# Kernel optimization log

Measured on AMD Instinct MI355X. Metric: run time of the kernel, lower is better.

The kernel has to match this reference:

```python
import jax, jax.numpy as jnp
import numpy as np

R = 0.4          # ball radius
K = 32           # max_neighbors
S = 512          # cluster_num
BN_EPS = 1e-5


def fps(data, npoint):
    """Furthest point sampling. data: [B,N,C] -> idx [B,npoint] int32.
    Deterministic start at index 0 (original uses randint)."""
    B, N, C = data.shape

    def step(carry, _):
        dist, far = carry
        cent = jnp.take_along_axis(data, far[:, None, None], axis=1)  # [B,1,C]
        d = jnp.sum((data - cent) ** 2, -1)                           # [B,N]
        dist = jnp.minimum(dist, d)
        new_far = jnp.argmax(dist, -1).astype(jnp.int32)
        return (dist, new_far), far

    dist0 = jnp.full((B, N), 1e10, data.dtype)
    far0 = jnp.zeros((B,), jnp.int32)
    _, idxs = jax.lax.scan(step, (dist0, far0), None, length=npoint)
    return idxs.T  # [B,npoint]


def gather_points(data, idx):
    """data [B,N,C], idx [B,S] -> [B,S,C]"""
    return jnp.take_along_axis(data, idx[..., None], axis=1)


def gather_groups(data, idx):
    """data [B,N,C], idx [B,S,K] -> [B,S,K,C]"""
    B, N, C = data.shape
    _, Sq, Kq = idx.shape
    flat = jnp.take_along_axis(data, idx.reshape(B, Sq * Kq)[..., None], axis=1)
    return flat.reshape(B, Sq, Kq, C)


def square_dist(a, b):
    """a [B,N,C], b [B,M,C] -> [B,N,M]"""
    return (-2.0 * jnp.einsum('bnc,bmc->bnm', a, b)
            + jnp.sum(a ** 2, -1)[:, :, None]
            + jnp.sum(b ** 2, -1)[:, None, :])


def knn_query(data, query, max_neighbors, r):
    """Ball query: indices of up to max_neighbors points within r, padded with
    the first valid index. data [B,N,C], query [B,S,C] -> [B,S,K] int32."""
    B, N, _ = data.shape
    d = square_dist(query, data)                              # [B,S,N]
    idx = jnp.where(d <= r * r, jnp.arange(N, dtype=jnp.int32)[None, None, :], N)
    idx = jnp.sort(idx, axis=-1)[:, :, :max_neighbors]        # ascending, N = invalid
    first = idx[:, :, :1]
    return jnp.where(idx == N, first, idx)


def mlp_layer(x, w, b, g, be):
    """1x1 Conv2d + BatchNorm2d (training-mode batch stats) + ReLU.
    x [B,S,K,Cin], w [Cout,Cin] -> [B,S,K,Cout]"""
    y = jnp.einsum('bskc,oc->bsko', x, w) + b
    m = jnp.mean(y, axis=(0, 1, 2))
    v = jnp.var(y, axis=(0, 1, 2))
    y = (y - m) * jax.lax.rsqrt(v + BN_EPS) * g + be
    return jax.nn.relu(y)


def setup_inputs() -> dict:
    key = jax.random.key(0)
    ks = jax.random.split(key, 5)
    B, N = 16, 8192
    data = jax.random.normal(ks[0], (B, N, 3), jnp.float32)
    data_feature = jax.random.normal(ks[1], (B, N, 3), jnp.float32)
    w0 = jax.random.normal(ks[2], (64, 6), jnp.float32) * 0.1
    w1 = jax.random.normal(ks[3], (64, 64), jnp.float32) * 0.1
    w2 = jax.random.normal(ks[4], (128, 64), jnp.float32) * 0.1
    zeros = lambda c: jnp.zeros((c,), jnp.float32)
    ones = lambda c: jnp.ones((c,), jnp.float32)
    return dict(data=data, data_feature=data_feature,
                w0=w0, b0=zeros(64), g0=ones(64), be0=zeros(64),
                w1=w1, b1=zeros(64), g1=ones(64), be1=zeros(64),
                w2=w2, b2=zeros(128), g2=ones(128), be2=zeros(128))


def reference(data, data_feature, w0, b0, g0, be0, w1, b1, g1, be1, w2, b2, g2, be2):
    B, N, C = data.shape
    fps_idx = fps(data, S)                              # [B,S]
    centroids = gather_points(data, fps_idx)            # [B,S,3]
    nbr_idx = knn_query(data, centroids, K, R)          # [B,S,K]
    sample = gather_groups(data, nbr_idx)               # [B,S,K,3]
    sample_norm = sample - centroids[:, :, None, :]
    feat = gather_groups(data_feature, nbr_idx)         # [B,S,K,3]
    x = jnp.concatenate([sample_norm, feat], axis=-1)   # [B,S,K,6]
    x = mlp_layer(x, w0, b0, g0, be0)
    x = mlp_layer(x, w1, b1, g1, be1)
    x = mlp_layer(x, w2, b2, g2, be2)
    out = jnp.max(x, axis=2)                            # [B,S,128]
    return centroids, out
```

## Files before the change

### kernel.cpp

```cpp
#include <hip/hip_runtime.h>
#include <math.h>

constexpr int Bc = 16;
constexpr int Nc = 8192;
constexpr int Sc = 512;
constexpr int Kc = 32;
constexpr int Pc = Bc * Sc * Kc;

typedef float v2f __attribute__((ext_vector_type(2)));

#if defined(__has_builtin)
#if __has_builtin(__builtin_elementwise_fma)
#define PKFMA(a, b, c) __builtin_elementwise_fma(a, b, c)
#endif
#endif
#ifndef PKFMA
__device__ __forceinline__ v2f pkfma_(v2f a, v2f b, v2f c) {
  v2f r; r.x = fmaf(a.x, b.x, c.x); r.y = fmaf(a.y, b.y, c.y); return r;
}
#define PKFMA(a, b, c) pkfma_(a, b, c)
#endif

template <int CTRL>
__device__ __forceinline__ float dpp_max_stage(float x) {
  int p = __builtin_amdgcn_update_dpp(0, __float_as_int(x), CTRL, 0xf, 0xf, true);
  return fmaxf(x, __int_as_float(p));
}

__global__ __launch_bounds__(256, 1)
void fps_kernel(const float* __restrict__ data,
                float* __restrict__ cent_out,
                float* __restrict__ cent_ws) {
  const int b = blockIdx.x;
  const int t = threadIdx.x;
  const int lane = t & 63, w = t >> 6;

  __shared__ float lx[Nc], ly[Nc], lz[Nc];
  __shared__ unsigned long long red_k[2][4];
  __shared__ int idx_hist[Sc];

  const float* db = data + (size_t)b * Nc * 3;

  float px[32], py[32], pz[32], dist[32];
#pragma unroll
  for (int j = 0; j < 32; ++j) {
    int p = t + 256 * j;
    px[j] = db[p * 3 + 0];
    py[j] = db[p * 3 + 1];
    pz[j] = db[p * 3 + 2];
    dist[j] = 1e10f;
    lx[p] = px[j]; ly[p] = py[j]; lz[p] = pz[j];
  }
  __syncthreads();

  int far = 0;
  for (int it = 0; it < Sc; ++it) {
    const int sfar = __builtin_amdgcn_readfirstlane(far);
    if (t == 0) idx_hist[it] = sfar;
    const float cx = lx[sfar];
    const float cy = ly[sfar];
    const float cz = lz[sfar];

    float best = -1.0f; int bj = 0;
#pragma unroll
    for (int j = 0; j < 32; ++j) {
      float dx = __fsub_rn(px[j], cx);
      float dy = __fsub_rn(py[j], cy);
      float dz = __fsub_rn(pz[j], cz);
      float d = __fadd_rn(__fadd_rn(__fmul_rn(dx, dx), __fmul_rn(dy, dy)),
                          __fmul_rn(dz, dz));
      float nd = fminf(dist[j], d);
      dist[j] = nd;
      if (nd > best) { best = nd; bj = j; }
    }
    const int bidx = t + 256 * bj;

    float wmax = best;
    wmax = dpp_max_stage<0xB1>(wmax);
    wmax = dpp_max_stage<0x4E>(wmax);
    wmax = dpp_max_stage<0x141>(wmax);
    wmax = dpp_max_stage<0x140>(wmax);
    wmax = fmaxf(wmax, __shfl_xor(wmax, 16));
    wmax = fmaxf(wmax, __shfl_xor(wmax, 32));

    unsigned long long m = __ballot(best == wmax);
    int idx;
    if (__popcll(m) == 1) {
      idx = __shfl(bidx, (int)__ffsll((long long)m) - 1);
    } else {
      int cand = (best == wmax) ? bidx : 0x7fffffff;
#pragma unroll
      for (int off = 32; off; off >>= 1) cand = min(cand, __shfl_xor(cand, off));
      idx = cand;
    }

    unsigned long long key =
        ((unsigned long long)__float_as_uint(wmax) << 32) |
        (unsigned long long)(0xFFFFFFFFu - (unsigned)idx);
    const int par = it & 1;
    if (lane == 0) red_k[par][w] = key;
    __syncthreads();

    unsigned long long k0 = red_k[par][0];
    unsigned long long k1 = red_k[par][1];
    unsigned long long k2 = red_k[par][2];
    unsigned long long k3 = red_k[par][3];
    unsigned long long ka = (k0 > k1) ? k0 : k1;
    unsigned long long kb = (k2 > k3) ? k2 : k3;
    unsigned long long kk = (ka > kb) ? ka : kb;
    far = (int)(0xFFFFFFFFu - (unsigned)(kk & 0xFFFFFFFFull));
  }

  __syncthreads();
  for (int s = t; s < Sc; s += 256) {
    int id = idx_hist[s];
    float vx = lx[id], vy = ly[id], vz = lz[id];
    size_t o = ((size_t)b * Sc + s) * 3;
    cent_out[o + 0] = vx; cent_out[o + 1] = vy; cent_out[o + 2] = vz;
    cent_ws[o + 0]  = vx; cent_ws[o + 1]  = vy; cent_ws[o + 2]  = vz;
  }
}

__global__ __launch_bounds__(256)
void ball_kernel(const float* __restrict__ data,
                 const float* __restrict__ feat,
                 const float* __restrict__ cent_ws,
                 const float* __restrict__ w0,
                 const float* __restrict__ b0,
                 float* __restrict__ x0,
                 float* __restrict__ part0) {
  const int w = threadIdx.x >> 6, lane = threadIdx.x & 63;
  const int t = threadIdx.x;
  const int q = blockIdx.x * 4 + w;
  const int b = q >> 9;
  const float* db = data + (size_t)b * Nc * 3;
  const float* fb = feat + (size_t)b * Nc * 3;

  const float qx = cent_ws[q * 3 + 0];
  const float qy = cent_ws[q * 3 + 1];
  const float qz = cent_ws[q * 3 + 2];
  const float q2 = __fadd_rn(__fadd_rn(__fmul_rn(qx, qx), __fmul_rn(qy, qy)),
                             __fmul_rn(qz, qz));

  __shared__ int nbr[4][Kc];
  __shared__ float x0s[6][128];
  int have = 0;
  for (int base = 0; base < Nc; base += 64) {
    int i = base + lane;
    float px = db[i * 3 + 0], py = db[i * 3 + 1], pz = db[i * 3 + 2];
    float p2 = __fadd_rn(__fadd_rn(__fmul_rn(px, px), __fmul_rn(py, py)),
                         __fmul_rn(pz, pz));
    float dt = fmaf(qz, pz, fmaf(qy, py, __fmul_rn(qx, px)));
    float d = __fadd_rn(__fadd_rn(__fmul_rn(-2.0f, dt), q2), p2);
    bool ok = d <= 0.16f;
    unsigned long long mask = __ballot(ok);
    if (mask) {
      int pos = have + __popcll(mask & ((1ull << lane) - 1ull));
      if (ok && pos < Kc) nbr[w][pos] = i;
      have += __popcll(mask);
      if (have >= Kc) break;
    }
  }
  if (have > Kc) have = Kc;
  __syncthreads();

  if (lane < Kc) {
    int k = lane;
    int j = nbr[w][k < have ? k : 0];
    float sx = __fsub_rn(db[j * 3 + 0], qx);
    float sy = __fsub_rn(db[j * 3 + 1], qy);
    float sz = __fsub_rn(db[j * 3 + 2], qz);
    float fx = fb[j * 3 + 0], fy = fb[j * 3 + 1], fz = fb[j * 3 + 2];
    size_t pidx = (size_t)q * Kc + k;
    x0[(size_t)0 * Pc + pidx] = sx;
    x0[(size_t)1 * Pc + pidx] = sy;
    x0[(size_t)2 * Pc + pidx] = sz;
    x0[(size_t)3 * Pc + pidx] = fx;
    x0[(size_t)4 * Pc + pidx] = fy;
    x0[(size_t)5 * Pc + pidx] = fz;
    int col = w * Kc + k;
    x0s[0][col] = sx; x0s[1][col] = sy; x0s[2][col] = sz;
    x0s[3][col] = fx; x0s[4][col] = fy; x0s[5][col] = fz;
  }
  __syncthreads();

  const int o = t & 63, q4 = t >> 6;
  float W[6];
#pragma unroll
  for (int c = 0; c < 6; ++c) W[c] = w0[o * 6 + c];
  const float bias = b0[o];
  float sum = 0.f, sq = 0.f;
#pragma unroll 4
  for (int k = 0; k < 32; ++k) {
    int p = q4 * 32 + k;
    float y = bias;
#pragma unroll
    for (int c = 0; c < 6; ++c) y = fmaf(x0s[c][p], W[c], y);
    sum += y;
    sq = fmaf(y, y, sq);
  }
  __shared__ float bsum[4][64], bsq[4][64];
  bsum[q4][o] = sum; bsq[q4][o] = sq;
  __syncthreads();
  if (t < 64)
    part0[blockIdx.x * 128 + t] =
        ((bsum[0][t] + bsum[1][t]) + bsum[2][t]) + bsum[3][t];
  else if (t < 128) {
    int oo = t - 64;
    part0[blockIdx.x * 128 + t] =
        ((bsq[0][oo] + bsq[1][oo]) + bsq[2][oo]) + bsq[3][oo];
  }
}

__global__ __launch_bounds__(256)
void reduce_k(const float* __restrict__ part, int nblk, int nch,
              const float* __restrict__ g, const float* __restrict__ be,
              float* __restrict__ AB) {
  const int o = blockIdx.x;
  const int t = threadIdx.x;
  double sum = 0.0, sq = 0.0;
  for (int i = t; i < nblk; i += 256) {
    sum += (double)part[(size_t)i * (2 * nch) + o];
    sq  += (double)part[(size_t)i * (2 * nch) + nch + o];
  }
  __shared__ double ls[256], lq[256];
  ls[t] = sum; lq[t] = sq;
  __syncthreads();
  for (int s = 128; s > 0; s >>= 1) {
    if (t < s) { ls[t] += ls[t + s]; lq[t] += lq[t + s]; }
    __syncthreads();
  }
  if (t == 0) {
    double m = ls[0] / (double)Pc;
    double v = lq[0] / (double)Pc - m * m;
    double A = (double)g[o] / sqrt(v + 1e-5);
    AB[o] = (float)A;
    AB[nch + o] = (float)((double)be[o] - m * A);
  }
}

__global__ __launch_bounds__(256)
void reduce2_final_k(const float* __restrict__ part, int nblk,
                     const float* __restrict__ g, const float* __restrict__ be,
                     const float* __restrict__ maxy2,
                     float* __restrict__ out) {
  const int o = blockIdx.x;
  const int t = threadIdx.x;
  double sum = 0.0, sq = 0.0;
  for (int i = t; i < nblk; i += 256) {
    sum += (double)part[(size_t)i * 256 + o];
    sq  += (double)part[(size_t)i * 256 + 128 + o];
  }
  __shared__ double ls[256], lq[256];
  ls[t] = sum; lq[t] = sq;
  __syncthreads();
  for (int s = 128; s > 0; s >>= 1) {
    if (t < s) { ls[t] += ls[t + s]; lq[t] += lq[t + s]; }
    __syncthreads();
  }
  __shared__ float sA, sB;
  if (t == 0) {
    double m = ls[0] / (double)Pc;
    double v = lq[0] / (double)Pc - m * m;
    double A = (double)g[o] / sqrt(v + 1e-5);
    sA = (float)A;
    sB = (float)((double)be[o] - m * A);
  }
  __syncthreads();
  const float A = sA, B = sB;
  for (int grp = t; grp < Bc * Sc; grp += 256) {
    float v = maxy2[(size_t)grp * 128 + o];
    out[(size_t)grp * 128 + o] = fmaxf(fmaf(v, A, B), 0.f);
  }
}

__global__ __launch_bounds__(256)
void pass_b(const float* __restrict__ x0, const float* __restrict__ w0,
            const float* __restrict__ b0, const float* __restrict__ AB0,
            const float* __restrict__ w1, const float* __restrict__ b1,
            float* __restrict__ y1, float* __restrict__ part1) {
  const int p = blockIdx.x * 256 + threadIdx.x;
  const int lane = threadIdx.x & 63, w = threadIdx.x >> 6;

  float xin[6];
#pragma unroll
  for (int c = 0; c < 6; ++c) xin[c] = x0[(size_t)c * Pc + p];

  float x1s[64];
#pragma unroll
  for (int o = 0; o < 64; ++o) {
    float y = b0[o];
#pragma unroll
    for (int c = 0; c < 6; ++c) y = fmaf(xin[c], w0[o * 6 + c], y);
    x1s[o] = fmaxf(fmaf(y, AB0[o], AB0[64 + o]), 0.f);
  }
  v2f x1p[32];
#pragma unroll
  for (int j = 0; j < 32; ++j) { x1p[j].x = x1s[2 * j]; x1p[j].y = x1s[2 * j + 1]; }

  const v2f* __restrict__ w1v = (const v2f*)w1;

  __shared__ float ssum[4][64][17], ssq[4][64][17];

  for (int o = 0; o < 64; ++o) {
    v2f a01; a01.x = b1[o]; a01.y = 0.f;
    v2f a23; a23.x = 0.f;   a23.y = 0.f;
#pragma unroll
    for (int c2 = 0; c2 < 32; c2 += 2) {
      a01 = PKFMA(x1p[c2 + 0], w1v[o * 32 + c2 + 0], a01);
      a23 = PKFMA(x1p[c2 + 1], w1v[o * 32 + c2 + 1], a23);
    }
    float acc = (a01.x + a01.y) + (a23.x + a23.y);
    y1[(size_t)o * Pc + p] = acc;

    float sv = acc + __shfl_xor(acc, 1);
    sv += __shfl_xor(sv, 2);
    float q = acc * acc;
    float qv = q + __shfl_xor(q, 1);
    qv += __shfl_xor(qv, 2);
    if ((lane & 3) == 0) {
      ssum[w][o][lane >> 2] = sv;
      ssq[w][o][lane >> 2] = qv;
    }
  }
  __syncthreads();
  if (threadIdx.x < 128) {
    const int o = threadIdx.x & 63;
    const bool isq = threadIdx.x >= 64;
    float s = 0.f;
#pragma unroll
    for (int ww = 0; ww < 4; ++ww)
      for (int k = 0; k < 16; ++k)
        s += isq ? ssq[ww][o][k] : ssum[ww][o][k];
    part1[blockIdx.x * 128 + threadIdx.x] = s;
  }
}

__global__ __launch_bounds__(256)
void pass_c(const float* __restrict__ y1, const float* __restrict__ AB1,
            const float* __restrict__ w2, const float* __restrict__ b2,
            float* __restrict__ maxy2, float* __restrict__ part2) {
  const int p = blockIdx.x * 256 + threadIdx.x;
  const int lane = threadIdx.x & 63, w = threadIdx.x >> 6;
  const int grp = p >> 5;

  v2f x2p[32];
#pragma unroll
  for (int c = 0; c < 64; c += 2) {
    float v0 = y1[(size_t)c * Pc + p];
    float v1 = y1[(size_t)(c + 1) * Pc + p];
    x2p[c >> 1].x = fmaxf(fmaf(v0, AB1[c], AB1[64 + c]), 0.f);
    x2p[c >> 1].y = fmaxf(fmaf(v1, AB1[c + 1], AB1[64 + c + 1]), 0.f);
  }

  const v2f* __restrict__ w2v = (const v2f*)w2;

  __shared__ float ssum[4][128][9], ssq[4][128][9];

  for (int o = 0; o < 128; ++o) {
    v2f a01; a01.x = b2[o]; a01.y = 0.f;
    v2f a23; a23.x = 0.f;   a23.y = 0.f;
#pragma unroll
    for (int c2 = 0; c2 < 32; c2 += 2) {
      a01 = PKFMA(x2p[c2 + 0], w2v[o * 32 + c2 + 0], a01);
      a23 = PKFMA(x2p[c2 + 1], w2v[o * 32 + c2 + 1], a23);
    }
    float acc = (a01.x + a01.y) + (a23.x + a23.y);

    float mx = acc;
#pragma unroll
    for (int off = 16; off > 0; off >>= 1) mx = fmaxf(mx, __shfl_xor(mx, off));
    if ((lane & 31) == 0) maxy2[(size_t)grp * 128 + o] = mx;

    float sv = acc + __shfl_xor(acc, 1);
    sv += __shfl_xor(sv, 2);
    sv += __shfl_xor(sv, 4);
    float q = acc * acc;
    float qv = q + __shfl_xor(q, 1);
    qv += __shfl_xor(qv, 2);
    qv += __shfl_xor(qv, 4);
    if ((lane & 7) == 0) {
      ssum[w][o][lane >> 3] = sv;
      ssq[w][o][lane >> 3] = qv;
    }
  }
  __syncthreads();
  {
    const int o = threadIdx.x & 127;
    const bool isq = threadIdx.x >= 128;
    float s = 0.f;
#pragma unroll
    for (int ww = 0; ww < 4; ++ww)
      for (int k = 0; k < 8; ++k)
        s += isq ? ssq[ww][o][k] : ssum[ww][o][k];
    part2[blockIdx.x * 256 + threadIdx.x] = s;
  }
}

extern "C" void kernel_launch(void* const* d_in, const int* in_sizes, int n_in,
                              void* d_out, int out_size, void* d_ws, size_t ws_size,
                              hipStream_t stream) {
  const float* data = (const float*)d_in[0];
  const float* feat = (const float*)d_in[1];
  const float* w0 = (const float*)d_in[2];
  const float* b0 = (const float*)d_in[3];
  const float* g0 = (const float*)d_in[4];
  const float* be0 = (const float*)d_in[5];
  const float* w1 = (const float*)d_in[6];
  const float* b1 = (const float*)d_in[7];
  const float* g1 = (const float*)d_in[8];
  const float* be1 = (const float*)d_in[9];
  const float* w2 = (const float*)d_in[10];
  const float* b2 = (const float*)d_in[11];
  const float* g2 = (const float*)d_in[12];
  const float* be2 = (const float*)d_in[13];
  float* out = (float*)d_out;

  float* ws = (float*)d_ws;
  float* cent_ws = ws; ws += (size_t)Bc * Sc * 3;
  float* x0 = ws;      ws += (size_t)6 * Pc;
  float* y1 = ws;      ws += (size_t)64 * Pc;
  float* maxy2 = ws;   ws += (size_t)Bc * Sc * 128;
  float* part0 = ws;   ws += 2048 * 128;
  float* part1 = ws;   ws += 1024 * 128;
  float* part2 = ws;   ws += 1024 * 256;
  float* AB0 = ws;     ws += 128;
  float* AB1 = ws;     ws += 128;

  fps_kernel<<<Bc, 256, 0, stream>>>(data, out, cent_ws);
  ball_kernel<<<(Bc * Sc) / 4, 256, 0, stream>>>(data, feat, cent_ws,
                                                 w0, b0, x0, part0);
  reduce_k<<<64, 256, 0, stream>>>(part0, 2048, 64, g0, be0, AB0);
  pass_b<<<Pc / 256, 256, 0, stream>>>(x0, w0, b0, AB0, w1, b1, y1, part1);
  reduce_k<<<64, 256, 0, stream>>>(part1, 1024, 64, g1, be1, AB1);
  pass_c<<<Pc / 256, 256, 0, stream>>>(y1, AB1, w2, b2, maxy2, part2);
  reduce2_final_k<<<128, 256, 0, stream>>>(part2, 1024, g2, be2, maxy2,
                                           out + (size_t)Bc * Sc * 3);
}
```

Measured before the change: 809.8 us.

## Fuse FPS and ball query into one kernel with flag-based producer-consumer overlap

Merges the furthest-point-sampling and ball-query/first-layer-stats kernels into one launch. Sixteen blocks run FPS and publish each chosen index to a global array initialised to -1. The other 240 blocks are persistent consumer waves that spin on those flags and run the ball query for each centroid as soon as it appears. This hides the long, serial FPS phase behind the ball query work and adds software prefetch of the next point chunk. The cost is spin-waiting, a dependence on all 256 blocks being co-resident (deadlock otherwise), and a changed partial-sum layout for the BN reduction.

```diff
diff --git a/kernel.cpp b/kernel.cpp
--- a/kernel.cpp
+++ b/kernel.cpp
@@ -6,6 +6,9 @@
 constexpr int Sc = 512;
 constexpr int Kc = 32;
 constexpr int Pc = Bc * Sc * Kc;
+
+constexpr int NBALL_BLK = 240;
+constexpr int NBALL_WAVES = NBALL_BLK * 4;
 
 typedef float v2f __attribute__((ext_vector_type(2)));
 
@@ -28,187 +31,194 @@
 }
 
 __global__ __launch_bounds__(256, 1)
-void fps_kernel(const float* __restrict__ data,
-                float* __restrict__ cent_out,
-                float* __restrict__ cent_ws) {
-  const int b = blockIdx.x;
-  const int t = threadIdx.x;
-  const int lane = t & 63, w = t >> 6;
-
+void fps_ball_fused(const float* __restrict__ data,
+                    const float* __restrict__ feat,
+                    const float* __restrict__ w0,
+                    const float* __restrict__ b0,
+                    int* __restrict__ idx_pub,
+                    float* __restrict__ cent_out,
+                    float* __restrict__ x0,
+                    float* __restrict__ part0) {
   __shared__ float lx[Nc], ly[Nc], lz[Nc];
   __shared__ unsigned long long red_k[2][4];
   __shared__ int idx_hist[Sc];
-
-  const float* db = data + (size_t)b * Nc * 3;
-
-  float px[32], py[32], pz[32], dist[32];
-#pragma unroll
-  for (int j = 0; j < 32; ++j) {
-    int p = t + 256 * j;
-    px[j] = db[p * 3 + 0];
-    py[j] = db[p * 3 + 1];
-    pz[j] = db[p * 3 + 2];
-    dist[j] = 1e10f;
-    lx[p] = px[j]; ly[p] = py[j]; lz[p] = pz[j];
-  }
-  __syncthreads();
-
-  int far = 0;
-  for (int it = 0; it < Sc; ++it) {
-    const int sfar = __builtin_amdgcn_readfirstlane(far);
-    if (t == 0) idx_hist[it] = sfar;
-    const float cx = lx[sfar];
-    const float cy = ly[sfar];
-    const float cz = lz[sfar];
-
-    float best = -1.0f; int bj = 0;
+  __shared__ int nbr[4][Kc];
+  __shared__ float x0s[4][6][Kc];
+
+  const int t = threadIdx.x;
+  const int lane = t & 63, w = t >> 6;
+
+  if (blockIdx.x < Bc) {
+    const int b = blockIdx.x;
+    const float* db = data + (size_t)b * Nc * 3;
+
+    float px[32], py[32], pz[32], dist[32];
 #pragma unroll
     for (int j = 0; j < 32; ++j) {
-      float dx = __fsub_rn(px[j], cx);
-      float dy = __fsub_rn(py[j], cy);
-      float dz = __fsub_rn(pz[j], cz);
-      float d = __fadd_rn(__fadd_rn(__fmul_rn(dx, dx), __fmul_rn(dy, dy)),
-                          __fmul_rn(dz, dz));
-      float nd = fminf(dist[j], d);
-      dist[j] = nd;
-      if (nd > best) { best = nd; bj = j; }
-    }
-    const int bidx = t + 256 * bj;
-
-    float wmax = best;
-    wmax = dpp_max_stage<0xB1>(wmax);
-    wmax = dpp_max_stage<0x4E>(wmax);
-    wmax = dpp_max_stage<0x141>(wmax);
-    wmax = dpp_max_stage<0x140>(wmax);
-    wmax = fmaxf(wmax, __shfl_xor(wmax, 16));
-    wmax = fmaxf(wmax, __shfl_xor(wmax, 32));
-
-    unsigned long long m = __ballot(best == wmax);
-    int idx;
-    if (__popcll(m) == 1) {
-      idx = __shfl(bidx, (int)__ffsll((long long)m) - 1);
-    } else {
-      int cand = (best == wmax) ? bidx : 0x7fffffff;
-#pragma unroll
-      for (int off = 32; off; off >>= 1) cand = min(cand, __shfl_xor(cand, off));
-      idx = cand;
-    }
-
-    unsigned long long key =
-        ((unsigned long long)__float_as_uint(wmax) << 32) |
-        (unsigned long long)(0xFFFFFFFFu - (unsigned)idx);
-    const int par = it & 1;
-    if (lane == 0) red_k[par][w] = key;
+      int p = t + 256 * j;
+      px[j] = db[p * 3 + 0];
+      py[j] = db[p * 3 + 1];
+      pz[j] = db[p * 3 + 2];
+      dist[j] = 1e10f;
+      lx[p] = px[j]; ly[p] = py[j]; lz[p] = pz[j];
+    }
     __syncthreads();
 
-    unsigned long long k0 = red_k[par][0];
-    unsigned long long k1 = red_k[par][1];
-    unsigned long long k2 = red_k[par][2];
-    unsigned long long k3 = red_k[par][3];
-    unsigned long long ka = (k0 > k1) ? k0 : k1;
-    unsigned long long kb = (k2 > k3) ? k2 : k3;
-    unsigned long long kk = (ka > kb) ? ka : kb;
-    far = (int)(0xFFFFFFFFu - (unsigned)(kk & 0xFFFFFFFFull));
-  }
-
-  __syncthreads();
-  for (int s = t; s < Sc; s += 256) {
-    int id = idx_hist[s];
-    float vx = lx[id], vy = ly[id], vz = lz[id];
-    size_t o = ((size_t)b * Sc + s) * 3;
-    cent_out[o + 0] = vx; cent_out[o + 1] = vy; cent_out[o + 2] = vz;
-    cent_ws[o + 0]  = vx; cent_ws[o + 1]  = vy; cent_ws[o + 2]  = vz;
-  }
-}
-
-__global__ __launch_bounds__(256)
-void ball_kernel(const float* __restrict__ data,
-                 const float* __restrict__ feat,
-                 const float* __restrict__ cent_ws,
-                 const float* __restrict__ w0,
-                 const float* __restrict__ b0,
-                 float* __restrict__ x0,
-                 float* __restrict__ part0) {
-  const int w = threadIdx.x >> 6, lane = threadIdx.x & 63;
-  const int t = threadIdx.x;
-  const int q = blockIdx.x * 4 + w;
-  const int b = q >> 9;
-  const float* db = data + (size_t)b * Nc * 3;
-  const float* fb = feat + (size_t)b * Nc * 3;
-
-  const float qx = cent_ws[q * 3 + 0];
-  const float qy = cent_ws[q * 3 + 1];
-  const float qz = cent_ws[q * 3 + 2];
-  const float q2 = __fadd_rn(__fadd_rn(__fmul_rn(qx, qx), __fmul_rn(qy, qy)),
-                             __fmul_rn(qz, qz));
-
-  __shared__ int nbr[4][Kc];
-  __shared__ float x0s[6][128];
-  int have = 0;
-  for (int base = 0; base < Nc; base += 64) {
-    int i = base + lane;
-    float px = db[i * 3 + 0], py = db[i * 3 + 1], pz = db[i * 3 + 2];
-    float p2 = __fadd_rn(__fadd_rn(__fmul_rn(px, px), __fmul_rn(py, py)),
-                         __fmul_rn(pz, pz));
-    float dt = fmaf(qz, pz, fmaf(qy, py, __fmul_rn(qx, px)));
-    float d = __fadd_rn(__fadd_rn(__fmul_rn(-2.0f, dt), q2), p2);
-    bool ok = d <= 0.16f;
-    unsigned long long mask = __ballot(ok);
-    if (mask) {
-      int pos = have + __popcll(mask & ((1ull << lane) - 1ull));
-      if (ok && pos < Kc) nbr[w][pos] = i;
-      have += __popcll(mask);
-      if (have >= Kc) break;
-    }
-  }
-  if (have > Kc) have = Kc;
-  __syncthreads();
-
-  if (lane < Kc) {
-    int k = lane;
-    int j = nbr[w][k < have ? k : 0];
-    float sx = __fsub_rn(db[j * 3 + 0], qx);
-    float sy = __fsub_rn(db[j * 3 + 1], qy);
-    float sz = __fsub_rn(db[j * 3 + 2], qz);
-    float fx = fb[j * 3 + 0], fy = fb[j * 3 + 1], fz = fb[j * 3 + 2];
-    size_t pidx = (size_t)q * Kc + k;
-    x0[(size_t)0 * Pc + pidx] = sx;
-    x0[(size_t)1 * Pc + pidx] = sy;
-    x0[(size_t)2 * Pc + pidx] = sz;
-    x0[(size_t)3 * Pc + pidx] = fx;
-    x0[(size_t)4 * Pc + pidx] = fy;
-    x0[(size_t)5 * Pc + pidx] = fz;
-    int col = w * Kc + k;
-    x0s[0][col] = sx; x0s[1][col] = sy; x0s[2][col] = sz;
-    x0s[3][col] = fx; x0s[4][col] = fy; x0s[5][col] = fz;
-  }
-  __syncthreads();
-
-  const int o = t & 63, q4 = t >> 6;
-  float W[6];
-#pragma unroll
-  for (int c = 0; c < 6; ++c) W[c] = w0[o * 6 + c];
-  const float bias = b0[o];
-  float sum = 0.f, sq = 0.f;
+    int far = 0;
+    for (int it = 0; it < Sc; ++it) {
+      const int sfar = __builtin_amdgcn_readfirstlane(far);
+      if (t == 0) {
+        idx_hist[it] = sfar;
+        atomicExch(&idx_pub[(b << 9) + it], sfar);
+      }
+      const float cx = lx[sfar];
+      const float cy = ly[sfar];
+      const float cz = lz[sfar];
+
+      float best = -1.0f; int bj = 0;
+#pragma unroll
+      for (int j = 0; j < 32; ++j) {
+        float dx = __fsub_rn(px[j], cx);
+        float dy = __fsub_rn(py[j], cy);
+        float dz = __fsub_rn(pz[j], cz);
+        float d = __fadd_rn(__fadd_rn(__fmul_rn(dx, dx), __fmul_rn(dy, dy)),
+                            __fmul_rn(dz, dz));
+        float nd = fminf(dist[j], d);
+        dist[j] = nd;
+        if (nd > best) { best = nd; bj = j; }
+      }
+      const int bidx = t + 256 * bj;
+
+      float wmax = best;
+      wmax = dpp_max_stage<0xB1>(wmax);
+      wmax = dpp_max_stage<0x4E>(wmax);
+      wmax = dpp_max_stage<0x141>(wmax);
+      wmax = dpp_max_stage<0x140>(wmax);
+      wmax = fmaxf(wmax, __shfl_xor(wmax, 16));
+      wmax = fmaxf(wmax, __shfl_xor(wmax, 32));
+
+      unsigned long long m = __ballot(best == wmax);
+      int idx;
+      if (__popcll(m) == 1) {
+        idx = __shfl(bidx, (int)__ffsll((long long)m) - 1);
+      } else {
+        int cand = (best == wmax) ? bidx : 0x7fffffff;
+#pragma unroll
+        for (int off = 32; off; off >>= 1) cand = min(cand, __shfl_xor(cand, off));
+        idx = cand;
+      }
+
+      unsigned long long key =
+          ((unsigned long long)__float_as_uint(wmax) << 32) |
+          (unsigned long long)(0xFFFFFFFFu - (unsigned)idx);
+      const int par = it & 1;
+      if (lane == 0) red_k[par][w] = key;
+      __syncthreads();
+
+      unsigned long long k0 = red_k[par][0];
+      unsigned long long k1 = red_k[par][1];
+      unsigned long long k2 = red_k[par][2];
+      unsigned long long k3 = red_k[par][3];
+      unsigned long long ka = (k0 > k1) ? k0 : k1;
+      unsigned long long kb = (k2 > k3) ? k2 : k3;
+      unsigned long long kk = (ka > kb) ? ka : kb;
+      far = (int)(0xFFFFFFFFu - (unsigned)(kk & 0xFFFFFFFFull));
+    }
+
+    __syncthreads();
+    for (int s = t; s < Sc; s += 256) {
+      int id = idx_hist[s];
+      size_t o = ((size_t)b * Sc + s) * 3;
+      cent_out[o + 0] = lx[id];
+      cent_out[o + 1] = ly[id];
+      cent_out[o + 2] = lz[id];
+    }
+  } else {
+    const int wid = (blockIdx.x - Bc) * 4 + w;
+    const int bb = wid & 15;
+    const int u  = wid >> 4;
+    const float* db = data + (size_t)bb * Nc * 3;
+    const float* fb = feat + (size_t)bb * Nc * 3;
+
+    float W[6];
+#pragma unroll
+    for (int c = 0; c < 6; ++c) W[c] = w0[lane * 6 + c];
+    const float bias = b0[lane];
+    float sum = 0.f, sq = 0.f;
+
+    for (int s = u; s < Sc; s += 60) {
+      const int q = bb * Sc + s;
+
+      float px = db[lane * 3 + 0];
+      float py = db[lane * 3 + 1];
+      float pz = db[lane * 3 + 2];
+
+      int ci;
+      for (;;) {
+        int t0 = -1;
+        if (lane == 0) t0 = atomicAdd(&idx_pub[q], 0);
+        ci = __shfl(t0, 0);
+        if (ci >= 0) break;
+        __builtin_amdgcn_s_sleep(32);
+      }
+
+      const float qx = db[ci * 3 + 0];
+      const float qy = db[ci * 3 + 1];
+      const float qz = db[ci * 3 + 2];
+      const float q2 = __fadd_rn(__fadd_rn(__fmul_rn(qx, qx), __fmul_rn(qy, qy)),
+                                 __fmul_rn(qz, qz));
+
+      int have = 0;
+      for (int base = 0; base < Nc; base += 64) {
+        const int inext = (base + 64 + lane) & (Nc - 1);
+        float nx = db[inext * 3 + 0];
+        float ny = db[inext * 3 + 1];
+        float nz = db[inext * 3 + 2];
+
+        float p2 = __fadd_rn(__fadd_rn(__fmul_rn(px, px), __fmul_rn(py, py)),
+                             __fmul_rn(pz, pz));
+        float dt = fmaf(qz, pz, fmaf(qy, py, __fmul_rn(qx, px)));
+        float d = __fadd_rn(__fadd_rn(__fmul_rn(-2.0f, dt), q2), p2);
+        bool ok = d <= 0.16f;
+        unsigned long long mask = __ballot(ok);
+        if (mask) {
+          int pos = have + __popcll(mask & ((1ull << lane) - 1ull));
+          if (ok && pos < Kc) nbr[w][pos] = base + lane;
+          have += __popcll(mask);
+          if (have >= Kc) break;
+        }
+        px = nx; py = ny; pz = nz;
+      }
+      if (have > Kc) have = Kc;
+
+      if (lane < Kc) {
+        int j = nbr[w][lane < have ? lane : 0];
+        float sx = __fsub_rn(db[j * 3 + 0], qx);
+        float sy = __fsub_rn(db[j * 3 + 1], qy);
+        float sz = __fsub_rn(db[j * 3 + 2], qz);
+        float fx = fb[j * 3 + 0], fy = fb[j * 3 + 1], fz = fb[j * 3 + 2];
+        size_t pidx = (size_t)q * Kc + lane;
+        x0[(size_t)0 * Pc + pidx] = sx;
+        x0[(size_t)1 * Pc + pidx] = sy;
+        x0[(size_t)2 * Pc + pidx] = sz;
+        x0[(size_t)3 * Pc + pidx] = fx;
+        x0[(size_t)4 * Pc + pidx] = fy;
+        x0[(size_t)5 * Pc + pidx] = fz;
+        x0s[w][0][lane] = sx; x0s[w][1][lane] = sy; x0s[w][2][lane] = sz;
+        x0s[w][3][lane] = fx; x0s[w][4][lane] = fy; x0s[w][5][lane] = fz;
+      }
+
 #pragma unroll 4
-  for (int k = 0; k < 32; ++k) {
-    int p = q4 * 32 + k;
-    float y = bias;
-#pragma unroll
-    for (int c = 0; c < 6; ++c) y = fmaf(x0s[c][p], W[c], y);
-    sum += y;
-    sq = fmaf(y, y, sq);
-  }
-  __shared__ float bsum[4][64], bsq[4][64];
-  bsum[q4][o] = sum; bsq[q4][o] = sq;
-  __syncthreads();
-  if (t < 64)
-    part0[blockIdx.x * 128 + t] =
-        ((bsum[0][t] + bsum[1][t]) + bsum[2][t]) + bsum[3][t];
-  else if (t < 128) {
-    int oo = t - 64;
-    part0[blockIdx.x * 128 + t] =
-        ((bsq[0][oo] + bsq[1][oo]) + bsq[2][oo]) + bsq[3][oo];
+      for (int k = 0; k < Kc; ++k) {
+        float y = bias;
+#pragma unroll
+        for (int c = 0; c < 6; ++c) y = fmaf(x0s[w][c][k], W[c], y);
+        sum += y;
+        sq = fmaf(y, y, sq);
+      }
+    }
+    part0[(size_t)wid * 128 + lane] = sum;
+    part0[(size_t)wid * 128 + 64 + lane] = sq;
   }
 }
 
@@ -417,20 +427,21 @@
   float* out = (float*)d_out;
 
   float* ws = (float*)d_ws;
-  float* cent_ws = ws; ws += (size_t)Bc * Sc * 3;
+  int* idx_pub = (int*)ws; ws += (size_t)Bc * Sc;
   float* x0 = ws;      ws += (size_t)6 * Pc;
   float* y1 = ws;      ws += (size_t)64 * Pc;
   float* maxy2 = ws;   ws += (size_t)Bc * Sc * 128;
-  float* part0 = ws;   ws += 2048 * 128;
+  float* part0 = ws;   ws += (size_t)NBALL_WAVES * 128;
   float* part1 = ws;   ws += 1024 * 128;
   float* part2 = ws;   ws += 1024 * 256;
   float* AB0 = ws;     ws += 128;
   float* AB1 = ws;     ws += 128;
 
-  fps_kernel<<<Bc, 256, 0, stream>>>(data, out, cent_ws);
-  ball_kernel<<<(Bc * Sc) / 4, 256, 0, stream>>>(data, feat, cent_ws,
-                                                 w0, b0, x0, part0);
-  reduce_k<<<64, 256, 0, stream>>>(part0, 2048, 64, g0, be0, AB0);
+  hipMemsetAsync(idx_pub, 0xFF, (size_t)Bc * Sc * sizeof(int), stream);
+
+  fps_ball_fused<<<Bc + NBALL_BLK, 256, 0, stream>>>(data, feat, w0, b0,
+                                                     idx_pub, out, x0, part0);
+  reduce_k<<<64, 256, 0, stream>>>(part0, NBALL_WAVES, 64, g0, be0, AB0);
   pass_b<<<Pc / 256, 256, 0, stream>>>(x0, w0, b0, AB0, w1, b1, y1, part1);
   reduce_k<<<64, 256, 0, stream>>>(part1, 1024, 64, g1, be1, AB1);
   pass_c<<<Pc / 256, 256, 0, stream>>>(y1, AB1, w2, b2, maxy2, part2);
```

Result: faster. 793.3 us (-2.0%).
